# Kernel tuning notes

Measured on AMD Instinct MI355X. Metric: run time of the kernel, lower is better.

The kernel has to match this reference:

```python
import jax, jax.numpy as jnp
import numpy as np
from jax import lax

B, S, K = 256, 2048, 16
E, KE, NI = 20, 17, 30


def crf_nll(emissions, mask, tags, transitions, start_transitions, end_transitions):
    """Mean negative log-likelihood of a linear-chain CRF (pytorch-crf/bert4torch math)."""
    dt = emissions.dtype
    maskf = mask.astype(dt)
    # ---- numerator: score of gold path ----
    em_tag = jnp.take_along_axis(emissions, tags[..., None], axis=2)[..., 0]  # [B,S]
    trans_step = transitions[tags[:, :-1], tags[:, 1:]]                        # [B,S-1]
    num = start_transitions[tags[:, 0]] + em_tag[:, 0]
    num = num + jnp.sum((trans_step + em_tag[:, 1:]) * maskf[:, 1:], axis=1)
    lengths = jnp.sum(mask.astype(jnp.int32), axis=1)                          # [B]
    last_tags = jnp.take_along_axis(tags, (lengths - 1)[:, None], axis=1)[:, 0]
    num = num + end_transitions[last_tags]
    # ---- denominator: log partition via forward algorithm (scan over time) ----
    alpha0 = start_transitions[None, :] + emissions[:, 0]                      # [B,K]

    def step(alpha, xs):
        em_t, m_t = xs                                                         # [B,K], [B]
        nxt = jax.nn.logsumexp(alpha[:, :, None] + transitions[None] + em_t[:, None, :], axis=1)
        alpha = jnp.where(m_t[:, None], nxt, alpha)
        return alpha, None

    alpha, _ = lax.scan(step, alpha0,
                        (emissions[:, 1:].swapaxes(0, 1), mask[:, 1:].swapaxes(0, 1)))
    logZ = jax.nn.logsumexp(alpha + end_transitions[None, :], axis=1)          # [B]
    return jnp.mean(logZ - num)


def cross_entropy_mean(logits, labels):
    logp = jax.nn.log_softmax(logits, axis=-1)
    nll = -jnp.take_along_axis(logp, labels[:, None], axis=1)[:, 0]
    return jnp.mean(nll)


def cross_entropy_ignore0(logits, labels):
    logp = jax.nn.log_softmax(logits, axis=-1)
    nll = -jnp.take_along_axis(logp, labels[:, None], axis=1)[:, 0]
    valid = (labels != 0).astype(logits.dtype)
    return jnp.sum(nll * valid) / jnp.maximum(jnp.sum(valid), 1.0)


def setup_inputs() -> dict:
    key = jax.random.key(0)
    ks = jax.random.split(key, 10)
    emission_score = jax.random.normal(ks[0], (B, S, K), dtype=jnp.float32)
    lengths = jax.random.randint(ks[1], (B,), S // 2, S + 1)
    attention_mask = jnp.arange(S)[None, :] < lengths[:, None]                 # bool [B,S]
    entity_logit = jax.random.normal(ks[2], (B, E, KE), dtype=jnp.float32)
    intent_logit = jax.random.normal(ks[3], (B, NI), dtype=jnp.float32)
    seq_labels = jax.random.randint(ks[4], (B, S), 0, K)
    entity_labels = jax.random.randint(ks[5], (B, E), 0, KE)
    intent_labels = jax.random.randint(ks[6], (B,), 0, NI)
    transitions = jax.random.normal(ks[7], (K, K), dtype=jnp.float32) * 0.1
    start_transitions = jax.random.normal(ks[8], (K,), dtype=jnp.float32) * 0.1
    end_transitions = jax.random.normal(ks[9], (K,), dtype=jnp.float32) * 0.1
    return {"emission_score": emission_score, "attention_mask": attention_mask,
            "entity_logit": entity_logit, "intent_logit": intent_logit,
            "seq_labels": seq_labels, "entity_labels": entity_labels,
            "intent_labels": intent_labels, "transitions": transitions,
            "start_transitions": start_transitions, "end_transitions": end_transitions}


def reference(emission_score, attention_mask, entity_logit, intent_logit,
              seq_labels, entity_labels, intent_labels,
              transitions, start_transitions, end_transitions):
    loss_i = cross_entropy_mean(intent_logit, intent_labels)
    loss_e1 = crf_nll(emission_score, attention_mask, seq_labels,
                      transitions, start_transitions, end_transitions)
    loss_e2 = cross_entropy_ignore0(entity_logit.reshape(-1, entity_logit.shape[-1]),
                                    entity_labels.reshape(-1))
    loss = (loss_e1 + loss_e2 + loss_i) / 3.0
    return (loss, loss_e1, loss_e2, loss_i)
```

## Files before the change

kernel.cpp:

```cpp
#include <hip/hip_runtime.h>
#include <hip/hip_bf16.h>

constexpr int B  = 256, S = 2048, K = 16;
constexpr int E  = 20, KE = 17, NI = 30;
constexpr int C  = 32;
constexpr int L  = S / C;

typedef float    f4 __attribute__((ext_vector_type(4)));
typedef short    s4 __attribute__((ext_vector_type(4)));
typedef unsigned u2 __attribute__((ext_vector_type(2)));

__device__ inline unsigned pk2_trunc(float a, float b) {
  return __builtin_amdgcn_perm(__float_as_uint(b), __float_as_uint(a),
                               0x07060302u);
}

#if __has_builtin(__builtin_amdgcn_mfma_f32_16x16x16bf16_1k)
__device__ inline f4 mfma16(s4 a, s4 b, f4 c) {
  return __builtin_amdgcn_mfma_f32_16x16x16bf16_1k(a, b, c, 0, 0, 0);
}
#else
__device__ inline f4 mfma16(s4 a, s4 b, f4 c) {
  f4 d;
  asm volatile("s_nop 1\n\t"
               "v_mfma_f32_16x16x16_bf16 %0, %1, %2, %3\n\t"
               "s_nop 7\n\ts_nop 7"
               : "=&v"(d) : "v"(a), "v"(b), "v"(c));
  return d;
}
#endif

__global__ __launch_bounds__(1024, 4) void k_fused(
    const float* __restrict__ em,
    const float* __restrict__ trans,
    const int* __restrict__ tags,
    const int* __restrict__ mask,
    const float* __restrict__ startT,
    const float* __restrict__ endT,
    const float* __restrict__ intent_logit,
    const int* __restrict__ intent_labels,
    const float* __restrict__ entity_logit,
    const int* __restrict__ entity_labels,
    float* __restrict__ rowCrf,
    float* __restrict__ rowInt,
    float* __restrict__ rowE2,
    float* __restrict__ rowCnt) {
  __shared__ float tl[256];
  __shared__ alignas(16) float stage[16 * 2048];
  __shared__ int   sigl[C];
  __shared__ float numl[16];
  __shared__ int   lenl[16];

  int tid = threadIdx.x;
  if (tid < 256) tl[tid] = trans[tid];
  __syncthreads();

  int w = tid >> 6, lane = tid & 63;
  int b  = blockIdx.x;
  int cA = w;
  int cB = 31 - w;
  int g4 = lane >> 4, j0 = lane & 15;

  int tloA = 1 + cA * L;
  int tloB = 1 + cB * L;
  int WB = min(L, S - tloB);

  float* stA = stage + w * 2048;
  float* stB = stA + 1024;

  {
    int tAs = tloA + lane;
    int tBs = tloB + min(lane, WB - 1);
    const float* gAs = em + ((size_t)b * S + tAs) * 16;
    const float* gBs = em + ((size_t)b * S + tBs) * 16;
#pragma unroll
    for (int q = 0; q < 4; ++q) {
      f4 va = *(const f4*)(gAs + 4 * q);
      f4 vb = *(const f4*)(gBs + 4 * q);
      f4 ea, eb;
      ea.x = __expf(va.x); ea.y = __expf(va.y);
      ea.z = __expf(va.z); ea.w = __expf(va.w);
      eb.x = __expf(vb.x); eb.y = __expf(vb.y);
      eb.z = __expf(vb.z); eb.w = __expf(vb.w);
      *(f4*)(stA + lane * 16 + 4 * q) = ea;
      *(f4*)(stB + lane * 16 + 4 * q) = eb;
    }
  }

  const int* mrow = mask + b * S;
  bool mvA = (mrow[tloA + lane] != 0);
  bool mvB = (lane < WB) && (mrow[tloB + lane] != 0);

  const int* trow = tags + b * S;
  int ttA = tloA + lane;
  int ttB = tloB + min(lane, WB - 1);
  int tacA = trow[ttA], tapA = trow[ttA - 1];
  int tacB = trow[ttB], tapB = trow[ttB - 1];
  float gAv = em[((size_t)b * S + ttA) * 16 + tacA];
  float gBv = em[((size_t)b * S + ttB) * 16 + tacB];

  int nA = __popcll(__ballot(mvA));
  int nB = __popcll(__ballot(mvB));

  float etF0 = __expf(tl[(4 * g4 + 0) * 16 + j0]);
  float etF1 = __expf(tl[(4 * g4 + 1) * 16 + j0]);
  float etF2 = __expf(tl[(4 * g4 + 2) * 16 + j0]);
  float etF3 = __expf(tl[(4 * g4 + 3) * 16 + j0]);
  float etT0 = __expf(tl[j0 * 16 + 4 * g4 + 0]);
  float etT1 = __expf(tl[j0 * 16 + 4 * g4 + 1]);
  float etT2 = __expf(tl[j0 * 16 + 4 * g4 + 2]);
  float etT3 = __expf(tl[j0 * 16 + 4 * g4 + 3]);

  f4 ID;
  ID.x = (4 * g4 + 0 == j0) ? 1.f : 0.f;
  ID.y = (4 * g4 + 1 == j0) ? 1.f : 0.f;
  ID.z = (4 * g4 + 2 == j0) ? 1.f : 0.f;
  ID.w = (4 * g4 + 3 == j0) ? 1.f : 0.f;
  f4 Y0A = ID, X1A = ID, X2A = ID, X3A = ID;
  f4 Y0B = ID, X1B = ID, X2B = ID, X3B = ID;
  int sigA = 0, sigB = 0;
  const f4 zero4 = {0.f, 0.f, 0.f, 0.f};

#define STEPF(st_, row_, ACC_)                                          \
  { float ee = (st_)[(row_) * 16 + j0];                                 \
    unsigned a01 = pk2_trunc(etF0 * ee, etF1 * ee);                     \
    unsigned a23 = pk2_trunc(etF2 * ee, etF3 * ee);                     \
    unsigned b01 = pk2_trunc(ACC_.x, ACC_.y);                           \
    unsigned b23 = pk2_trunc(ACC_.z, ACC_.w);                           \
    ACC_ = mfma16(__builtin_bit_cast(s4, (u2){a01, a23}),               \
                  __builtin_bit_cast(s4, (u2){b01, b23}), zero4); }
#define STEPB(st_, row_, ACC_)                                          \
  { f4 ev = *(const f4*)((st_) + (row_) * 16 + 4 * g4);                 \
    unsigned a01 = pk2_trunc(etT0 * ev.x, etT1 * ev.y);                 \
    unsigned a23 = pk2_trunc(etT2 * ev.z, etT3 * ev.w);                 \
    unsigned b01 = pk2_trunc(ACC_.x, ACC_.y);                           \
    unsigned b23 = pk2_trunc(ACC_.z, ACC_.w);                           \
    ACC_ = mfma16(__builtin_bit_cast(s4, (u2){a01, a23}),               \
                  __builtin_bit_cast(s4, (u2){b01, b23}), zero4); }
#define RES(ACC_, SIG_)                                                 \
  { unsigned fb = __builtin_amdgcn_readfirstlane(__float_as_uint(ACC_.x));\
    int e = (int)((fb >> 23) & 0xffu) - 127;                            \
    e = max(min(e, 126), -126);                                         \
    float sc = __uint_as_float((unsigned)(127 - e) << 23);              \
    ACC_.x *= sc; ACC_.y *= sc; ACC_.z *= sc; ACC_.w *= sc;             \
    SIG_ += e; }
#define OPC(U_, V_, OUT_)                                               \
  { unsigned ua = pk2_trunc(U_.x, U_.y), ub = pk2_trunc(U_.z, U_.w);    \
    unsigned va = pk2_trunc(V_.x, V_.y), vb = pk2_trunc(V_.z, V_.w);    \
    OUT_ = mfma16(__builtin_bit_cast(s4, (u2){ua, ub}),                 \
                  __builtin_bit_cast(s4, (u2){va, vb}), zero4); }

#pragma unroll
  for (int u = 0; u < 16; ++u) {
    STEPF(stA, u, Y0A)
    if (u < nB) STEPF(stB, u, Y0B)
    STEPB(stA, 31 - u, X1A)
    if (31 - u < nB) STEPB(stB, 31 - u, X1B)
    STEPB(stA, 47 - u, X2A)
    if (47 - u < nB) STEPB(stB, 47 - u, X2B)
    if (63 - u < nA) STEPB(stA, 63 - u, X3A)
    if (63 - u < nB) STEPB(stB, 63 - u, X3B)
    if (u == 7 || u == 15) {
      RES(Y0A, sigA) RES(X1A, sigA) RES(X2A, sigA) RES(X3A, sigA)
      RES(Y0B, sigB) RES(X1B, sigB) RES(X2B, sigB) RES(X3B, sigB)
    }
  }

  f4 oA, pA, MA, oB, pB, MB;
  OPC(X1A, Y0A, oA) RES(oA, sigA)
  OPC(X2A, oA,  pA) RES(pA, sigA)
  OPC(X3A, pA,  MA) RES(MA, sigA)
  OPC(X1B, Y0B, oB) RES(oB, sigB)
  OPC(X2B, oB,  pB) RES(pB, sigB)
  OPC(X3B, pB,  MB) RES(MB, sigB)
#undef STEPF
#undef STEPB
#undef RES
#undef OPC

  float numc = 0.f;
  if (lane < nA) numc += tl[tapA * 16 + tacA] + gAv;
  if (lane < nB) numc += tl[tapB * 16 + tacB] + gBv;
#pragma unroll
  for (int o = 1; o < 64; o <<= 1) numc += __shfl_xor(numc, o);

  __syncthreads();

  float* Ml = stage;
  int base = (j0 >> 2) * 64 + 16 * g4 + (j0 & 3);
  float* moA = &Ml[cA * 256];
  moA[base + 0]  = MA.x;
  moA[base + 4]  = MA.y;
  moA[base + 8]  = MA.z;
  moA[base + 12] = MA.w;
  float* moB = &Ml[cB * 256];
  moB[base + 0]  = MB.x;
  moB[base + 4]  = MB.y;
  moB[base + 8]  = MB.z;
  moB[base + 12] = MB.w;
  if (lane == 0) {
    sigl[cA] = sigA;
    sigl[cB] = sigB;
    numl[w]  = numc;
    lenl[w]  = nA + nB + (cA == 0 ? 1 : 0);
  }
  __syncthreads();

  if (w == 0) {
    int l = lane, jb = l & 15, ib = l >> 4;

    float numtot = (l < 16) ? numl[l] : 0.f;
    int   lentot = (l < 16) ? lenl[l] : 0;
#pragma unroll
    for (int o = 1; o < 16; o <<= 1) {
      numtot += __shfl_xor(numtot, o);
      lentot += __shfl_xor(lentot, o);
    }

    const float* erow = em + (size_t)b * S * 16;
    float a0v = startT[jb] + erow[jb];
    float m0 = a0v;
#pragma unroll
    for (int o = 1; o < 16; o <<= 1) m0 = fmaxf(m0, __shfl_xor(m0, o));
    float v = __expf(a0v - m0);
    float total = m0;
    int tg0 = tags[(size_t)b * S];
    float num0 = __shfl(a0v, tg0);

    int sv = (l < C) ? sigl[l] : 0;
    const f4* mptr = (const f4*)stage;
    f4 p0 = mptr[0 * 64 + l], p1 = mptr[1 * 64 + l];
    f4 p2 = mptr[2 * 64 + l], p3 = mptr[3 * 64 + l];

#define PROC(p_, c_)                                                         \
    {                                                                        \
      float v0 = __shfl(v, 4 * ib + 0), v1 = __shfl(v, 4 * ib + 1);          \
      float v2 = __shfl(v, 4 * ib + 2), v3 = __shfl(v, 4 * ib + 3);          \
      float sacc = v0 * p_.x + v1 * p_.y + v2 * p_.z + v3 * p_.w;            \
      sacc += __shfl_xor(sacc, 16); sacc += __shfl_xor(sacc, 32);            \
      float mx = sacc;                                                       \
      for (int o = 1; o < 16; o <<= 1) mx = fmaxf(mx, __shfl_xor(mx, o));    \
      int e = (int)((__float_as_uint(mx) >> 23) & 0xffu) - 127;              \
      e = max(min(e, 126), -126);                                            \
      float sc = __uint_as_float((unsigned)(127 - e) << 23);                 \
      v = sacc * sc;                                                         \
      total += (float)(__shfl(sv, (c_)) + e) * 0.6931471805599453f;          \
    }

    for (int cc = 0; cc < C; cc += 4) {
      PROC(p0, cc + 0) if (cc + 4 < C) p0 = mptr[(cc + 4) * 64 + l];
      PROC(p1, cc + 1) if (cc + 4 < C) p1 = mptr[(cc + 5) * 64 + l];
      PROC(p2, cc + 2) if (cc + 4 < C) p2 = mptr[(cc + 6) * 64 + l];
      PROC(p3, cc + 3) if (cc + 4 < C) p3 = mptr[(cc + 7) * 64 + l];
    }
#undef PROC

    float term = v * __expf(endT[jb]);
#pragma unroll
    for (int o = 1; o < 16; o <<= 1) term += __shfl_xor(term, o);
    if (l == 0) {
      float logZ = __logf(term) + total;
      float numb = numtot + num0 + endT[tags[(size_t)b * S + lentot - 1]];
      rowCrf[b] = logZ - numb;
    }
  } else if (w == 1) {
    int l = lane;
    const float* row = intent_logit + b * NI;
    float x = (l < NI) ? row[l] : -1e30f;
    float mi = x;
#pragma unroll
    for (int o = 1; o < 64; o <<= 1) mi = fmaxf(mi, __shfl_xor(mi, o));
    float se = (l < NI) ? __expf(x - mi) : 0.f;
#pragma unroll
    for (int o = 1; o < 64; o <<= 1) se += __shfl_xor(se, o);

    float nll2 = 0.f, cnt2 = 0.f;
    if (l < E) {
      const float* er = entity_logit + (size_t)(b * E + l) * KE;
      float me = -1e30f;
      for (int k = 0; k < KE; ++k) me = fmaxf(me, er[k]);
      float ss = 0.f;
      for (int k = 0; k < KE; ++k) ss += __expf(er[k] - me);
      int lb = entity_labels[b * E + l];
      if (lb != 0) { nll2 = -(er[lb] - me - __logf(ss)); cnt2 = 1.f; }
    }
#pragma unroll
    for (int o = 1; o < 64; o <<= 1) {
      nll2 += __shfl_xor(nll2, o);
      cnt2 += __shfl_xor(cnt2, o);
    }
    if (l == 0) {
      int lab = intent_labels[b];
      rowInt[b] = -(row[lab] - mi - __logf(se));
      rowE2[b]  = nll2;
      rowCnt[b] = cnt2;
    }
  }
}

__global__ __launch_bounds__(256) void k_final(const float* __restrict__ rowCrf,
                                               const float* __restrict__ rowInt,
                                               const float* __restrict__ rowE2,
                                               const float* __restrict__ rowCnt,
                                               float* __restrict__ out) {
  int tid = threadIdx.x;
  float s0 = rowCrf[tid], s1 = rowInt[tid], s2 = rowE2[tid], s3 = rowCnt[tid];
  __shared__ float r[4][4];
#pragma unroll
  for (int o = 32; o; o >>= 1) {
    s0 += __shfl_down(s0, o); s1 += __shfl_down(s1, o);
    s2 += __shfl_down(s2, o); s3 += __shfl_down(s3, o);
  }
  if ((tid & 63) == 0) {
    r[tid >> 6][0] = s0; r[tid >> 6][1] = s1;
    r[tid >> 6][2] = s2; r[tid >> 6][3] = s3;
  }
  __syncthreads();
  if (tid == 0) {
    float crf = r[0][0] + r[1][0] + r[2][0] + r[3][0];
    float it  = r[0][1] + r[1][1] + r[2][1] + r[3][1];
    float e2  = r[0][2] + r[1][2] + r[2][2] + r[3][2];
    float cn  = r[0][3] + r[1][3] + r[2][3] + r[3][3];
    float le1 = crf / (float)B;
    float li  = it  / (float)B;
    float le2 = e2 / fmaxf(cn, 1.f);
    out[0] = (le1 + le2 + li) / 3.f;
    out[1] = le1;
    out[2] = le2;
    out[3] = li;
  }
}

extern "C" void kernel_launch(void* const* d_in, const int* in_sizes, int n_in,
                              void* d_out, int out_size, void* d_ws, size_t ws_size,
                              hipStream_t stream) {
  const float* em            = (const float*)d_in[0];
  const int*   mask          = (const int*)  d_in[1];
  const float* entity_logit  = (const float*)d_in[2];
  const float* intent_logit  = (const float*)d_in[3];
  const int*   seq_labels    = (const int*)  d_in[4];
  const int*   entity_labels = (const int*)  d_in[5];
  const int*   intent_labels = (const int*)  d_in[6];
  const float* trans         = (const float*)d_in[7];
  const float* startT        = (const float*)d_in[8];
  const float* endT          = (const float*)d_in[9];
  float* out = (float*)d_out;

  char* ws = (char*)d_ws;
  float* rowCrf = (float*)ws;
  float* rowInt = (float*)(ws + 1024);
  float* rowE2  = (float*)(ws + 2048);
  float* rowCnt = (float*)(ws + 3072);

  k_fused<<<B, 1024, 0, stream>>>(em, trans, seq_labels, mask, startT, endT,
                                  intent_logit, intent_labels,
                                  entity_logit, entity_labels,
                                  rowCrf, rowInt, rowE2, rowCnt);
  k_final<<<1, 256, 0, stream>>>(rowCrf, rowInt, rowE2, rowCnt, out);
}
```

Measured before the change: 32.07 us.

## Chain CRF chunk transfer products with one 32x32 block-diagonal MFMA per step

Replaces the 16x16 MFMA scheme, which split each chunk into four sub-chains and combined them at the end, with a single sequential chain per chunk. Each step issues one 32x32x16 bf16 MFMA that holds both of the wave's chunks as block-diagonal halves, and v_permlane32_swap moves the output back into operand layout. Emissions are loaded straight from global into registers, triple-buffered and prefetched one group ahead, and exponentiated per step. This drops the 128KB LDS staging buffer and its barrier, which should allow higher occupancy. In exchange the dependent MFMA chain becomes 64 steps long with no independent work to overlap, and accumulating bf16 truncation over that chain may cost accuracy.

```diff
diff --git a/kernel.cpp b/kernel.cpp
--- a/kernel.cpp
+++ b/kernel.cpp
@@ -6,29 +6,23 @@
 constexpr int C  = 32;
 constexpr int L  = S / C;
 
-typedef float    f4 __attribute__((ext_vector_type(4)));
-typedef short    s4 __attribute__((ext_vector_type(4)));
-typedef unsigned u2 __attribute__((ext_vector_type(2)));
+typedef float    f4  __attribute__((ext_vector_type(4)));
+typedef float    f16v __attribute__((ext_vector_type(16)));
+typedef short    s8  __attribute__((ext_vector_type(8)));
+typedef unsigned u4  __attribute__((ext_vector_type(4)));
 
 __device__ inline unsigned pk2_trunc(float a, float b) {
   return __builtin_amdgcn_perm(__float_as_uint(b), __float_as_uint(a),
                                0x07060302u);
 }
 
-#if __has_builtin(__builtin_amdgcn_mfma_f32_16x16x16bf16_1k)
-__device__ inline f4 mfma16(s4 a, s4 b, f4 c) {
-  return __builtin_amdgcn_mfma_f32_16x16x16bf16_1k(a, b, c, 0, 0, 0);
-}
-#else
-__device__ inline f4 mfma16(s4 a, s4 b, f4 c) {
-  f4 d;
-  asm volatile("s_nop 1\n\t"
-               "v_mfma_f32_16x16x16_bf16 %0, %1, %2, %3\n\t"
-               "s_nop 7\n\ts_nop 7"
-               : "=&v"(d) : "v"(a), "v"(b), "v"(c));
-  return d;
-}
-#endif
+__device__ inline void plswap(unsigned& a, unsigned& b) {
+  asm volatile("v_permlane32_swap_b32 %0, %1" : "+v"(a), "+v"(b));
+}
+
+__device__ inline f16v mfma32(s8 a, s8 b, f16v c) {
+  return __builtin_amdgcn_mfma_f32_32x32x16_bf16(a, b, c, 0, 0, 0);
+}
 
 __global__ __launch_bounds__(1024, 4) void k_fused(
     const float* __restrict__ em,
@@ -46,7 +40,7 @@
     float* __restrict__ rowE2,
     float* __restrict__ rowCnt) {
   __shared__ float tl[256];
-  __shared__ alignas(16) float stage[16 * 2048];
+  __shared__ alignas(16) float Ml[C * 256];
   __shared__ int   sigl[C];
   __shared__ float numl[16];
   __shared__ int   lenl[16];
@@ -59,33 +53,27 @@
   int b  = blockIdx.x;
   int cA = w;
   int cB = 31 - w;
-  int g4 = lane >> 4, j0 = lane & 15;
+
+  int lam = lane & 31, lh = lane >> 5, r15 = lane & 15;
+  bool Ah = lam < 16;
 
   int tloA = 1 + cA * L;
   int tloB = 1 + cB * L;
   int WB = min(L, S - tloB);
 
-  float* stA = stage + w * 2048;
-  float* stB = stA + 1024;
-
-  {
-    int tAs = tloA + lane;
-    int tBs = tloB + min(lane, WB - 1);
-    const float* gAs = em + ((size_t)b * S + tAs) * 16;
-    const float* gBs = em + ((size_t)b * S + tBs) * 16;
-#pragma unroll
-    for (int q = 0; q < 4; ++q) {
-      f4 va = *(const f4*)(gAs + 4 * q);
-      f4 vb = *(const f4*)(gBs + 4 * q);
-      f4 ea, eb;
-      ea.x = __expf(va.x); ea.y = __expf(va.y);
-      ea.z = __expf(va.z); ea.w = __expf(va.w);
-      eb.x = __expf(vb.x); eb.y = __expf(vb.y);
-      eb.z = __expf(vb.z); eb.w = __expf(vb.w);
-      *(f4*)(stA + lane * 16 + 4 * q) = ea;
-      *(f4*)(stB + lane * 16 + 4 * q) = eb;
-    }
-  }
+  int cme   = Ah ? cA : cB;
+  int tloMe = 1 + cme * L;
+  int Wme   = min(L, S - tloMe);
+  const float* gP = em + ((size_t)b * S + tloMe) * 16 + r15;
+
+  float f0[8], f1[8], f2[8];
+#define LDG(bf_, g_)                                                    \
+  { _Pragma("unroll")                                                   \
+    for (int u = 0; u < 8; ++u)                                         \
+      bf_[u] = gP[16 * min(8 * (g_) + u, Wme - 1)]; }
+
+  LDG(f0, 0)
+  LDG(f1, 1)
 
   const int* mrow = mask + b * S;
   bool mvA = (mrow[tloA + lane] != 0);
@@ -102,81 +90,93 @@
   int nA = __popcll(__ballot(mvA));
   int nB = __popcll(__ballot(mvB));
 
-  float etF0 = __expf(tl[(4 * g4 + 0) * 16 + j0]);
-  float etF1 = __expf(tl[(4 * g4 + 1) * 16 + j0]);
-  float etF2 = __expf(tl[(4 * g4 + 2) * 16 + j0]);
-  float etF3 = __expf(tl[(4 * g4 + 3) * 16 + j0]);
-  float etT0 = __expf(tl[j0 * 16 + 4 * g4 + 0]);
-  float etT1 = __expf(tl[j0 * 16 + 4 * g4 + 1]);
-  float etT2 = __expf(tl[j0 * 16 + 4 * g4 + 2]);
-  float etT3 = __expf(tl[j0 * 16 + 4 * g4 + 3]);
-
-  f4 ID;
-  ID.x = (4 * g4 + 0 == j0) ? 1.f : 0.f;
-  ID.y = (4 * g4 + 1 == j0) ? 1.f : 0.f;
-  ID.z = (4 * g4 + 2 == j0) ? 1.f : 0.f;
-  ID.w = (4 * g4 + 3 == j0) ? 1.f : 0.f;
-  f4 Y0A = ID, X1A = ID, X2A = ID, X3A = ID;
-  f4 Y0B = ID, X1B = ID, X2B = ID, X3B = ID;
+  float ek0 = __expf(tl[(8 * lh + 0) * 16 + r15]);
+  float ek1 = __expf(tl[(8 * lh + 1) * 16 + r15]);
+  float ek2 = __expf(tl[(8 * lh + 2) * 16 + r15]);
+  float ek3 = __expf(tl[(8 * lh + 3) * 16 + r15]);
+  float ek4 = __expf(tl[(8 * lh + 4) * 16 + r15]);
+  float ek5 = __expf(tl[(8 * lh + 5) * 16 + r15]);
+  float ek6 = __expf(tl[(8 * lh + 6) * 16 + r15]);
+  float ek7 = __expf(tl[(8 * lh + 7) * 16 + r15]);
+
+  unsigned idb0 = ((8 * lh + 0 == r15) ? 0x3F80u : 0u) |
+                  ((8 * lh + 1 == r15) ? 0x3F800000u : 0u);
+  unsigned idb1 = ((8 * lh + 2 == r15) ? 0x3F80u : 0u) |
+                  ((8 * lh + 3 == r15) ? 0x3F800000u : 0u);
+  unsigned idb2 = ((8 * lh + 4 == r15) ? 0x3F80u : 0u) |
+                  ((8 * lh + 5 == r15) ? 0x3F800000u : 0u);
+  unsigned idb3 = ((8 * lh + 6 == r15) ? 0x3F80u : 0u) |
+                  ((8 * lh + 7 == r15) ? 0x3F800000u : 0u);
+
+  unsigned bw0 = idb0, bw1 = idb1, bw2 = idb2, bw3 = idb3;
+  f16v d;
+  const f16v zero16 = {0.f,0.f,0.f,0.f,0.f,0.f,0.f,0.f,
+                       0.f,0.f,0.f,0.f,0.f,0.f,0.f,0.f};
   int sigA = 0, sigB = 0;
-  const f4 zero4 = {0.f, 0.f, 0.f, 0.f};
-
-#define STEPF(st_, row_, ACC_)                                          \
-  { float ee = (st_)[(row_) * 16 + j0];                                 \
-    unsigned a01 = pk2_trunc(etF0 * ee, etF1 * ee);                     \
-    unsigned a23 = pk2_trunc(etF2 * ee, etF3 * ee);                     \
-    unsigned b01 = pk2_trunc(ACC_.x, ACC_.y);                           \
-    unsigned b23 = pk2_trunc(ACC_.z, ACC_.w);                           \
-    ACC_ = mfma16(__builtin_bit_cast(s4, (u2){a01, a23}),               \
-                  __builtin_bit_cast(s4, (u2){b01, b23}), zero4); }
-#define STEPB(st_, row_, ACC_)                                          \
-  { f4 ev = *(const f4*)((st_) + (row_) * 16 + 4 * g4);                 \
-    unsigned a01 = pk2_trunc(etT0 * ev.x, etT1 * ev.y);                 \
-    unsigned a23 = pk2_trunc(etT2 * ev.z, etT3 * ev.w);                 \
-    unsigned b01 = pk2_trunc(ACC_.x, ACC_.y);                           \
-    unsigned b23 = pk2_trunc(ACC_.z, ACC_.w);                           \
-    ACC_ = mfma16(__builtin_bit_cast(s4, (u2){a01, a23}),               \
-                  __builtin_bit_cast(s4, (u2){b01, b23}), zero4); }
-#define RES(ACC_, SIG_)                                                 \
-  { unsigned fb = __builtin_amdgcn_readfirstlane(__float_as_uint(ACC_.x));\
-    int e = (int)((fb >> 23) & 0xffu) - 127;                            \
-    e = max(min(e, 126), -126);                                         \
-    float sc = __uint_as_float((unsigned)(127 - e) << 23);              \
-    ACC_.x *= sc; ACC_.y *= sc; ACC_.z *= sc; ACC_.w *= sc;             \
-    SIG_ += e; }
-#define OPC(U_, V_, OUT_)                                               \
-  { unsigned ua = pk2_trunc(U_.x, U_.y), ub = pk2_trunc(U_.z, U_.w);    \
-    unsigned va = pk2_trunc(V_.x, V_.y), vb = pk2_trunc(V_.z, V_.w);    \
-    OUT_ = mfma16(__builtin_bit_cast(s4, (u2){ua, ub}),                 \
-                  __builtin_bit_cast(s4, (u2){va, vb}), zero4); }
-
-#pragma unroll
-  for (int u = 0; u < 16; ++u) {
-    STEPF(stA, u, Y0A)
-    if (u < nB) STEPF(stB, u, Y0B)
-    STEPB(stA, 31 - u, X1A)
-    if (31 - u < nB) STEPB(stB, 31 - u, X1B)
-    STEPB(stA, 47 - u, X2A)
-    if (47 - u < nB) STEPB(stB, 47 - u, X2B)
-    if (63 - u < nA) STEPB(stA, 63 - u, X3A)
-    if (63 - u < nB) STEPB(stB, 63 - u, X3B)
-    if (u == 7 || u == 15) {
-      RES(Y0A, sigA) RES(X1A, sigA) RES(X2A, sigA) RES(X3A, sigA)
-      RES(Y0B, sigB) RES(X1B, sigB) RES(X2B, sigB) RES(X3B, sigB)
-    }
-  }
-
-  f4 oA, pA, MA, oB, pB, MB;
-  OPC(X1A, Y0A, oA) RES(oA, sigA)
-  OPC(X2A, oA,  pA) RES(pA, sigA)
-  OPC(X3A, pA,  MA) RES(MA, sigA)
-  OPC(X1B, Y0B, oB) RES(oB, sigB)
-  OPC(X2B, oB,  pB) RES(pB, sigB)
-  OPC(X3B, pB,  MB) RES(MB, sigB)
-#undef STEPF
-#undef STEPB
-#undef RES
-#undef OPC
+
+#define STEPT(bf_, u_, s_)                                              \
+  {                                                                     \
+    float ee = __expf(bf_[u_]);                                         \
+    unsigned a0 = pk2_trunc(ek0 * ee, ek1 * ee);                        \
+    unsigned a1 = pk2_trunc(ek2 * ee, ek3 * ee);                        \
+    unsigned a2 = pk2_trunc(ek4 * ee, ek5 * ee);                        \
+    unsigned a3 = pk2_trunc(ek6 * ee, ek7 * ee);                        \
+    bool idMe = Ah ? ((s_) >= nA) : ((s_) >= nB);                       \
+    if (idMe) { a0 = idb0; a1 = idb1; a2 = idb2; a3 = idb3; }           \
+    u4 aw = {a0, a1, a2, a3};                                           \
+    u4 bwv = {bw0, bw1, bw2, bw3};                                      \
+    d = mfma32(__builtin_bit_cast(s8, aw),                              \
+               __builtin_bit_cast(s8, bwv), zero16);                    \
+  }
+#define PACK                                                            \
+  {                                                                     \
+    float v0 = Ah ? d[0] : d[8],  v1 = Ah ? d[1] : d[9];                \
+    float v2 = Ah ? d[2] : d[10], v3 = Ah ? d[3] : d[11];               \
+    float v4 = Ah ? d[4] : d[12], v5 = Ah ? d[5] : d[13];               \
+    float v6 = Ah ? d[6] : d[14], v7 = Ah ? d[7] : d[15];               \
+    unsigned Q  = pk2_trunc(v0, v1), Q2 = pk2_trunc(v2, v3);            \
+    unsigned P  = pk2_trunc(v4, v5), P2 = pk2_trunc(v6, v7);            \
+    plswap(Q, P); plswap(Q2, P2);                                       \
+    bw0 = Q; bw1 = Q2; bw2 = P; bw3 = P2;                               \
+  }
+#define RESCALE                                                         \
+  {                                                                     \
+    unsigned fa = (unsigned)__builtin_amdgcn_readlane(                  \
+        (int)__float_as_uint(d[0]), 0);                                 \
+    unsigned fb2 = (unsigned)__builtin_amdgcn_readlane(                 \
+        (int)__float_as_uint(d[8]), 16);                                \
+    int eA = (int)((fa >> 23) & 0xffu) - 127;                           \
+    int eB = (int)((fb2 >> 23) & 0xffu) - 127;                          \
+    eA = max(min(eA, 126), -126);                                       \
+    eB = max(min(eB, 126), -126);                                       \
+    float scAf = __uint_as_float((unsigned)(127 - eA) << 23);           \
+    float scBf = __uint_as_float((unsigned)(127 - eB) << 23);           \
+    float sc = Ah ? scAf : scBf;                                        \
+    d[0]*=sc; d[1]*=sc; d[2]*=sc; d[3]*=sc;                             \
+    d[4]*=sc; d[5]*=sc; d[6]*=sc; d[7]*=sc;                             \
+    d[8]*=sc; d[9]*=sc; d[10]*=sc; d[11]*=sc;                           \
+    d[12]*=sc; d[13]*=sc; d[14]*=sc; d[15]*=sc;                         \
+    sigA += eA; sigB += eB;                                             \
+  }
+#define GRP(bf_, g_)                                                    \
+  STEPT(bf_,0,8*(g_)+0) PACK  STEPT(bf_,1,8*(g_)+1) PACK                \
+  STEPT(bf_,2,8*(g_)+2) PACK  STEPT(bf_,3,8*(g_)+3) PACK                \
+  STEPT(bf_,4,8*(g_)+4) PACK  STEPT(bf_,5,8*(g_)+5) PACK                \
+  STEPT(bf_,6,8*(g_)+6) PACK  STEPT(bf_,7,8*(g_)+7) RESCALE PACK
+
+  LDG(f2, 2)  GRP(f0, 0)
+  LDG(f0, 3)  GRP(f1, 1)
+  LDG(f1, 4)  GRP(f2, 2)
+  LDG(f2, 5)  GRP(f0, 3)
+  LDG(f0, 6)  GRP(f1, 4)
+  LDG(f1, 7)  GRP(f2, 5)
+              GRP(f0, 6)
+              GRP(f1, 7)
+#undef GRP
+#undef LDG
+#undef STEPT
+#undef PACK
+#undef RESCALE
 
   float numc = 0.f;
   if (lane < nA) numc += tl[tapA * 16 + tacA] + gAv;
@@ -184,20 +184,15 @@
 #pragma unroll
   for (int o = 1; o < 64; o <<= 1) numc += __shfl_xor(numc, o);
 
-  __syncthreads();
-
-  float* Ml = stage;
-  int base = (j0 >> 2) * 64 + 16 * g4 + (j0 & 3);
-  float* moA = &Ml[cA * 256];
-  moA[base + 0]  = MA.x;
-  moA[base + 4]  = MA.y;
-  moA[base + 8]  = MA.z;
-  moA[base + 12] = MA.w;
-  float* moB = &Ml[cB * 256];
-  moB[base + 0]  = MB.x;
-  moB[base + 4]  = MB.y;
-  moB[base + 8]  = MB.z;
-  moB[base + 12] = MB.w;
+  {
+    float* mo = &Ml[(Ah ? cA : cB) * 256];
+    int colb = (r15 >> 2) * 64 + (r15 & 3);
+#define ST(u_)                                                          \
+    { int lr = ((u_) & 3) + 8 * ((u_) >> 2) + 4 * lh;                   \
+      mo[colb + 16 * (lr >> 2) + 4 * (lr & 3)] = Ah ? d[u_] : d[8 + (u_)]; }
+    ST(0) ST(1) ST(2) ST(3) ST(4) ST(5) ST(6) ST(7)
+#undef ST
+  }
   if (lane == 0) {
     sigl[cA] = sigA;
     sigl[cB] = sigB;
@@ -228,7 +223,7 @@
     float num0 = __shfl(a0v, tg0);
 
     int sv = (l < C) ? sigl[l] : 0;
-    const f4* mptr = (const f4*)stage;
+    const f4* mptr = (const f4*)Ml;
     f4 p0 = mptr[0 * 64 + l], p1 = mptr[1 * 64 + l];
     f4 p2 = mptr[2 * 64 + l], p3 = mptr[3 * 64 + l];
 
```

Result: slower. 37.49 us (+16.9%).
